# Kernel optimization log

Hardware: AMD Instinct MI355X
Metric: run time of the kernel (lower is better)

Reference implementation:

```python
import jax, jax.numpy as jnp
import numpy as np

B, T, C, H, N = 2, 1024, 2048, 32, 64
LAYER_ID, N_LAYERS = 12, 24
EPS = 1e-5 * 8 ** 2  # GroupNorm eps = 1e-5 * head_size_divisor**2


def setup_inputs() -> dict:
    key = jax.random.key(0)
    ks = jax.random.split(key, 16)
    nrm = lambda i, shape, s: jax.random.normal(ks[i], shape, jnp.float32) * s
    r01 = LAYER_ID / (N_LAYERS - 1)
    r1a0 = 1.0 - LAYER_ID / N_LAYERS
    ddd = (jnp.arange(C, dtype=jnp.float32) / C)[None, None, :]
    nn_ = jnp.arange(C, dtype=jnp.float32) / (C - 1)
    decay_speed = -7.0 + 5.0 * nn_ ** (0.85 + r01 ** 0.5)
    lin_s = 1.0 / float(np.sqrt(C))
    inp = dict(
        x=nrm(0, (B, T, C), 1.0),
        v_first=nrm(1, (B, T, C), 1.0),
        shift_state=jnp.zeros((B, C), jnp.float32),
        wkv_state=jnp.zeros((B, H, N, N), jnp.float32),
        x_r=1.0 - ddd ** (0.2 * r1a0),
        x_w=1.0 - ddd ** (0.9 * r1a0),
        x_k=1.0 - (ddd ** (0.9 * r1a0) + 0.4 * r01),
        x_v=1.0 - (ddd ** (0.4 * r1a0) + 0.6 * r01),
        x_a=1.0 - ddd ** (0.9 * r1a0),
        x_g=1.0 - ddd ** (0.2 * r1a0),
        w0=decay_speed[None, None, :] + 0.5,
        w1=nrm(2, (C, 64), 0.05), w2=nrm(3, (64, C), 0.1),
        a0=jnp.zeros((1, 1, C), jnp.float32),
        a1=nrm(4, (C, 64), 0.05), a2=nrm(5, (64, C), 0.1),
        v0=jnp.ones((1, 1, C), jnp.float32),
        v1=nrm(6, (C, 32), 0.05), v2=nrm(7, (32, C), 0.1),
        g1=nrm(8, (C, 128), 0.05), g2=nrm(9, (128, C), 0.1),
        k_k=jnp.full((1, 1, C), 0.85, jnp.float32),
        k_a=jnp.ones((1, 1, C), jnp.float32),
        r_k=nrm(10, (H, N), 0.02),
        W_r=nrm(11, (C, C), lin_s), W_k=nrm(12, (C, C), lin_s),
        W_v=nrm(13, (C, C), lin_s), W_o=nrm(14, (C, C), lin_s),
        ln_w=jnp.ones((C,), jnp.float32), ln_b=jnp.zeros((C,), jnp.float32),
    )
    return inp


def _forward(x, v_first, shift_state, wkv_state, x_r, x_w, x_k, x_v, x_a, x_g,
             w0, w1, w2, a0, a1, a2, v0, v1, v2, g1, g2, k_k, k_a, r_k,
             W_r, W_k, W_v, W_o, ln_w, ln_b):
    # token shift
    xx = jnp.concatenate([shift_state[:, None, :], x[:, :-1]], axis=1) - x
    xr, xw, xk, xv, xa, xg = (x + xx * m for m in (x_r, x_w, x_k, x_v, x_a, x_g))
    r = xr @ W_r
    k = xk @ W_k
    v = xv @ W_v
    # log-decay (strictly negative)
    w_log = -jax.nn.softplus(-(w0 + jnp.tanh(xw @ w1) @ w2)) - 0.5
    # residual value mixing towards layer-0 v (layer_id > 0 branch)
    v = v + (v_first - v) * jax.nn.sigmoid(v0 + xv @ v1 @ v2)
    a = jax.nn.sigmoid(a0 + xa @ a1 @ a2)
    g = jax.nn.sigmoid(xg @ g1) @ g2
    # per-head L2-normalized removal key
    kk = (k * k_k).reshape(B, T, H, N)
    kk = kk / jnp.maximum(jnp.linalg.norm(kk, axis=-1, keepdims=True), 1e-12)
    k2 = k * (1.0 + (a - 1.0) * k_a)
    # time-major [T,B,H,N] for the scan
    tm = lambda t: t.reshape(B, T, H, N).transpose(1, 0, 2, 3)
    rs, ks_, vs = tm(r), tm(k2), tm(v)
    ws = jnp.exp(tm(w_log))               # per-channel decay in (0,1)
    a_in = -kk.transpose(1, 0, 2, 3)      # removal direction
    b_in = (kk * a.reshape(B, T, H, N)).transpose(1, 0, 2, 3)
    def step(S, t):  # S: [B,H,Nv,Nk]
        r_, k_, v_, w_, a_, b_ = t
        sa = jnp.einsum('bhvk,bhk->bhv', S, a_)
        S = S * w_[:, :, None, :] \
            + jnp.einsum('bhv,bhk->bhvk', sa, b_) \
            + jnp.einsum('bhv,bhk->bhvk', v_, k_)
        return S, jnp.einsum('bhvk,bhk->bhv', S, r_)
    S_final, o = jax.lax.scan(step, wkv_state, (rs, ks_, vs, ws, a_in, b_in))
    o = o.transpose(1, 0, 2, 3)           # [B,T,H,N]
    # GroupNorm with H groups over C channels (per-head normalization)
    mu = o.mean(-1, keepdims=True)
    var = ((o - mu) ** 2).mean(-1, keepdims=True)
    on = ((o - mu) / jnp.sqrt(var + EPS)).reshape(B, T, C) * ln_w + ln_b
    # rkv bonus term
    rr, kr, vr = r.reshape(B, T, H, N), k2.reshape(B, T, H, N), v.reshape(B, T, H, N)
    bonus = ((rr * kr * r_k).sum(-1, keepdims=True) * vr).reshape(B, T, C)
    out = ((on + bonus) * g) @ W_o
    return out


def reference(x, v_first, shift_state, wkv_state, x_r, x_w, x_k, x_v, x_a, x_g,
              w0, w1, w2, a0, a1, a2, v0, v1, v2, g1, g2, k_k, k_a, r_k,
              W_r, W_k, W_v, W_o, ln_w, ln_b):
    return _forward(x, v_first, shift_state, wkv_state, x_r, x_w, x_k, x_v, x_a, x_g,
                    w0, w1, w2, a0, a1, a2, v0, v1, v2, g1, g2, k_k, k_a, r_k,
                    W_r, W_k, W_v, W_o, ln_w, ln_b)
```

## Files before the change

kernel.cpp:

```cpp
#include <hip/hip_runtime.h>
#include <cstdint>
#include <cstddef>


#define DI __device__ __forceinline__
static constexpr int T_ = 1024, C_ = 2048, H_ = 32;

typedef __attribute__((ext_vector_type(8))) __bf16 bf16x8;
typedef __attribute__((ext_vector_type(4))) float f32x4;
typedef __attribute__((ext_vector_type(8))) unsigned short us8v;
typedef __attribute__((ext_vector_type(4))) unsigned short us4v;
typedef __attribute__((ext_vector_type(2))) unsigned short us2v;

DI float sig_(float z) { return 1.0f / (1.0f + expf(-z)); }

DI unsigned short f2bf(float f) {
  union { float f; uint32_t u; } v; v.f = f;
  uint32_t u = v.u;
  return (unsigned short)((u + 0x7FFFu + ((u >> 16) & 1u)) >> 16);
}
DI float bf2f(unsigned short h) {
  union { uint32_t u; float f; } v; v.u = ((uint32_t)h) << 16;
  return v.f;
}

DI float dpp_xor1_add(float x) {
  int r = __builtin_amdgcn_update_dpp(0, __float_as_int(x), 0xB1, 0xF, 0xF, true);
  return x + __int_as_float(r);
}
DI float dpp_xor2_add(float x) {
  int r = __builtin_amdgcn_update_dpp(0, __float_as_int(x), 0x4E, 0xF, 0xF, true);
  return x + __int_as_float(r);
}
DI float dpp_hm_add(float x) {
  int r = __builtin_amdgcn_update_dpp(0, __float_as_int(x), 0x141, 0xF, 0xF, true);
  return x + __int_as_float(r);
}
DI float dpp_mir_add(float x) {
  int r = __builtin_amdgcn_update_dpp(0, __float_as_int(x), 0x140, 0xF, 0xF, true);
  return x + __int_as_float(r);
}

DI void gload16(const float* g, float* l) {
  __builtin_amdgcn_global_load_lds(
      (const __attribute__((address_space(1))) uint32_t*)g,
      (__attribute__((address_space(3))) uint32_t*)l, 16, 0, 0);
}
DI void gload16u(const unsigned short* g, unsigned short* l) {
  __builtin_amdgcn_global_load_lds(
      (const __attribute__((address_space(1))) uint32_t*)g,
      (__attribute__((address_space(3))) uint32_t*)l, 16, 0, 0);
}
DI void gload4(const float* g, float* l) {
  __builtin_amdgcn_global_load_lds(
      (const __attribute__((address_space(1))) uint32_t*)g,
      (__attribute__((address_space(3))) uint32_t*)l, 4, 0, 0);
}

struct Job {
  const float* A; const float* W; float* C; const float* bias;
  const float* mixv; const float* x; const float* shift;
  int N, K, ntn, aact, epi, tile_end;
};
struct Jobs { Job j[7]; };

__global__ __launch_bounds__(256) void gemm_oracle(Jobs P) {
  __shared__ float As[64][33];
  __shared__ float Ws[32][65];
  int bx = blockIdx.x, ji = 0;
  while (bx >= P.j[ji].tile_end) ++ji;
  Job J = P.j[ji];
  int tix = bx - (ji ? P.j[ji - 1].tile_end : 0);
  int mt = tix / J.ntn, nt = tix % J.ntn;
  int m0 = mt * 64, n0 = nt * 64;
  int tid = threadIdx.x, tx = tid & 15, ty = tid >> 4;
  float acc[4][4] = {};
  for (int k0 = 0; k0 < J.K; k0 += 32) {
    #pragma unroll
    for (int p = 0; p < 8; ++p) {
      int idx = p * 256 + tid;
      int r = idx >> 5, kc = idx & 31;
      int m = m0 + r, k = k0 + kc;
      float a;
      if (J.mixv) {
        float xv = J.x[(size_t)m * C_ + k];
        int t = m & (T_ - 1);
        float xp = (t == 0) ? J.shift[(size_t)(m >> 10) * C_ + k]
                            : J.x[(size_t)(m - 1) * C_ + k];
        a = xv + (xp - xv) * J.mixv[k];
      } else {
        a = J.A[(size_t)m * J.K + k];
        if (J.aact == 1) a = tanhf(a);
        else if (J.aact == 2) a = sig_(a);
      }
      As[r][kc] = a;
    }
    #pragma unroll
    for (int p = 0; p < 8; ++p) {
      int idx = p * 256 + tid;
      int kr = idx >> 6, nc = idx & 63;
      int n = n0 + nc;
      Ws[kr][nc] = (n < J.N) ? J.W[(size_t)(k0 + kr) * J.N + n] : 0.0f;
    }
    __syncthreads();
    #pragma unroll 4
    for (int kc = 0; kc < 32; ++kc) {
      float av[4], bv[4];
      #pragma unroll
      for (int i = 0; i < 4; ++i) av[i] = As[ty * 4 + i][kc];
      #pragma unroll
      for (int jn = 0; jn < 4; ++jn) bv[jn] = Ws[kc][tx * 4 + jn];
      #pragma unroll
      for (int i = 0; i < 4; ++i)
        #pragma unroll
        for (int jn = 0; jn < 4; ++jn) acc[i][jn] += av[i] * bv[jn];
    }
    __syncthreads();
  }
  #pragma unroll
  for (int i = 0; i < 4; ++i) {
    int rw = m0 + ty * 4 + i;
    #pragma unroll
    for (int jn = 0; jn < 4; ++jn) {
      int col = n0 + tx * 4 + jn;
      if (col < J.N) {
        float v = acc[i][jn];
        if (J.epi == 1) v = sig_(J.bias[col] + v);
        else if (J.epi == 2) v = 0.60653065971263342f * sig_(J.bias[col] + v);
        if (J.epi == 3) ((unsigned short*)J.C)[(size_t)rw * J.N + col] = f2bf(v);
        else            J.C[(size_t)rw * J.N + col] = v;
      }
    }
  }
}

struct TJob { const float* src; unsigned short* dh; unsigned short* dl; int N, ntn, tile_end; };
struct TJobs { TJob j[8]; };

__global__ __launch_bounds__(256) void wtrans(TJobs P) {
  __shared__ float t[64][65];
  int bx = blockIdx.x, ji = 0;
  while (bx >= P.j[ji].tile_end) ++ji;
  TJob J = P.j[ji];
  int tix = bx - (ji ? P.j[ji - 1].tile_end : 0);
  int kt = tix / J.ntn, nt = tix % J.ntn;
  int k0 = kt * 64, n0 = nt * 64;
  int tid = threadIdx.x;
  #pragma unroll
  for (int p = 0; p < 16; ++p) {
    int flat = p * 256 + tid;
    int r = flat >> 6, c = flat & 63;
    int n = n0 + c;
    t[r][c] = (n < J.N) ? J.src[(size_t)(k0 + r) * J.N + n] : 0.0f;
  }
  __syncthreads();
  #pragma unroll
  for (int p = 0; p < 8; ++p) {
    int flat = p * 256 + tid;
    int rr = flat >> 5, cc = (flat & 31) * 2;
    if (n0 + rr < J.N) {
      float w0v = t[cc][rr], w1v = t[cc + 1][rr];
      unsigned short h0 = f2bf(w0v), h1 = f2bf(w1v);
      us2v oh, ol;
      oh.x = h0; oh.y = h1;
      ol.x = f2bf(w0v - bf2f(h0));
      ol.y = f2bf(w1v - bf2f(h1));
      size_t off = (size_t)(n0 + rr) * 2048 + k0 + cc;
      *(us2v*)(J.dh + off) = oh;
      *(us2v*)(J.dl + off) = ol;
    }
  }
}

struct GJob {
  const float* A; const unsigned short* Wh; const unsigned short* Wl; float* C;
  const float* mixv; const float* shift;
  int N, K, ntn, kbeg, kend, atomicC, tile_end;
};
struct GJobs { GJob j[8]; };

__global__ __launch_bounds__(256, 2) void gemm_w256(GJobs P) {
  __shared__ unsigned short Ash[128][40];
  __shared__ unsigned short Asl[128][40];
  __shared__ unsigned short Bsh[256][32];
  __shared__ unsigned short Bsl[256][32];
  int bx = blockIdx.x, ji = 0;
  while (bx >= P.j[ji].tile_end) ++ji;
  GJob J = P.j[ji];
  int tix = bx - (ji ? P.j[ji - 1].tile_end : 0);
  int mt = tix / J.ntn, nt = tix % J.ntn;
  int m0 = mt * 128, n0 = nt * 256;
  int tid = threadIdx.x;
  int lane = tid & 63, wid = tid >> 6;
  int wr = wid >> 1, wc = wid & 1;
  int l15 = lane & 15, lg = lane >> 4;
  f32x4 acc[4][8] = {};

  int sr = tid >> 3, skq = tid & 7;
  float ax[4][4], aq[4][4], amv[4];

  auto loadA = [&](int k0) {
    int kk = k0 + skq * 4;
    if (J.mixv) *(float4*)amv = *(const float4*)(J.mixv + kk);
    #pragma unroll
    for (int p = 0; p < 4; ++p) {
      int m = m0 + p * 32 + sr;
      const float* xp0 = J.A + (size_t)m * J.K + kk;
      *(float4*)ax[p] = *(const float4*)xp0;
      if (J.mixv) {
        const float* pp = ((m & (T_ - 1)) == 0)
            ? (J.shift + (size_t)(m >> 10) * C_ + kk)
            : (xp0 - C_);
        *(float4*)aq[p] = *(const float4*)pp;
      }
    }
  };
  auto writeA = [&]() {
    #pragma unroll
    for (int p = 0; p < 4; ++p) {
      us4v oh, ol;
      #pragma unroll
      for (int q = 0; q < 4; ++q) {
        float va = J.mixv ? (ax[p][q] + (aq[p][q] - ax[p][q]) * amv[q]) : ax[p][q];
        unsigned short hq = f2bf(va);
        oh[q] = hq;
        ol[q] = f2bf(va - bf2f(hq));
      }
      int r = p * 32 + sr;
      *(us4v*)&Ash[r][skq * 4] = oh;
      *(us4v*)&Asl[r][skq * 4] = ol;
    }
  };
  auto stageB = [&](int k0) {
    #pragma unroll
    for (int j = 0; j < 4; ++j) {
      int r0 = wid * 64 + j * 16;
      int rdst = r0 + (lane >> 2);
      int nrow = n0 + rdst;
      if (nrow >= J.N) nrow = J.N - 1;
      int ssrc = (lane & 3) ^ ((rdst >> 1) & 3);
      size_t gofs = (size_t)nrow * J.K + k0 + ssrc * 8;
      gload16u(J.Wh + gofs, &Bsh[r0][0]);
      gload16u(J.Wl + gofs, &Bsl[r0][0]);
    }
  };

  loadA(J.kbeg);
  stageB(J.kbeg);
  writeA();
  asm volatile("s_waitcnt vmcnt(0)" ::: "memory");
  __syncthreads();

  for (int k0 = J.kbeg; k0 < J.kend; k0 += 32) {
    bool more = (k0 + 32 < J.kend);
    if (more) loadA(k0 + 32);
    bf16x8 afh[4], afl[4];
    #pragma unroll
    for (int i = 0; i < 4; ++i) {
      int rr = wr * 64 + i * 16 + l15;
      afh[i] = __builtin_bit_cast(bf16x8, *(const us8v*)&Ash[rr][lg * 8]);
      afl[i] = __builtin_bit_cast(bf16x8, *(const us8v*)&Asl[rr][lg * 8]);
    }
    #pragma unroll
    for (int jn = 0; jn < 8; ++jn) {
      int rb = wc * 128 + jn * 16 + l15;
      int sl = (lg ^ ((rb >> 1) & 3)) * 8;
      bf16x8 bh = __builtin_bit_cast(bf16x8, *(const us8v*)&Bsh[rb][sl]);
      bf16x8 bl = __builtin_bit_cast(bf16x8, *(const us8v*)&Bsl[rb][sl]);
      #pragma unroll
      for (int i = 0; i < 4; ++i) {
        acc[i][jn] = __builtin_amdgcn_mfma_f32_16x16x32_bf16(afh[i], bh, acc[i][jn], 0, 0, 0);
        acc[i][jn] = __builtin_amdgcn_mfma_f32_16x16x32_bf16(afl[i], bh, acc[i][jn], 0, 0, 0);
        acc[i][jn] = __builtin_amdgcn_mfma_f32_16x16x32_bf16(afh[i], bl, acc[i][jn], 0, 0, 0);
      }
    }
    __syncthreads();
    if (more) { stageB(k0 + 32); writeA(); }
    asm volatile("s_waitcnt vmcnt(0)" ::: "memory");
    __syncthreads();
  }

  int orow0 = m0 + wr * 64 + 4 * lg;
  int ocol0 = n0 + wc * 128 + l15;
  #pragma unroll
  for (int i = 0; i < 4; ++i) {
    #pragma unroll
    for (int jn = 0; jn < 8; ++jn) {
      int col = ocol0 + jn * 16;
      if (col < J.N) {
        #pragma unroll
        for (int rr = 0; rr < 4; ++rr) {
          size_t idx = (size_t)(orow0 + i * 16 + rr) * J.N + col;
          float v = acc[i][jn][rr];
          if (J.atomicC) atomicAdd(&J.C[idx], v);
          else           J.C[idx] = v;
        }
      }
    }
  }
}

__global__ __launch_bounds__(256) void prescan(
    float* __restrict__ kio, float* __restrict__ vio,
    float* __restrict__ amat_ain, float* __restrict__ vmix_bin,
    const float* __restrict__ vfirst,
    const float* __restrict__ k_k, const float* __restrict__ k_a) {
  int gh = blockIdx.x * 4 + (threadIdx.x >> 6);
  int lane = threadIdx.x & 63;
  int h = gh & (H_ - 1);
  size_t base = (size_t)gh * 64 + lane;
  int cc = h * 64 + lane;
  float kv = kio[base];
  float kkv = kv * k_k[cc];
  float ss = kkv * kkv;
  ss += __shfl_xor(ss, 1);  ss += __shfl_xor(ss, 2);  ss += __shfl_xor(ss, 4);
  ss += __shfl_xor(ss, 8);  ss += __shfl_xor(ss, 16); ss += __shfl_xor(ss, 32);
  float nrm = fmaxf(sqrtf(ss), 1e-12f);
  float kkn = kkv / nrm;
  float av = amat_ain[base];
  float vmv = vmix_bin[base];
  float vv = vio[base];
  kio[base] = kv * (1.0f + (av - 1.0f) * k_a[cc]);
  vio[base] = vv + (vfirst[base] - vv) * vmv;
  amat_ain[base] = -kkn;
  vmix_bin[base] = kkn * av;
}

static constexpr int CH = 8;
static constexpr int SEG = 512, WU = 96;

#define LOADSTEP(BUF, S_, Aa, Ww, Kk, Bb, Rr, Vt)                  \
  {                                                                \
    *(float4*)&Aa[0] = *(const float4*)&lds[BUF][3][S_][kb];       \
    *(float4*)&Ww[0] = *(const float4*)&lds[BUF][2][S_][kb];       \
    *(float4*)&Kk[0] = *(const float4*)&lds[BUF][1][S_][kb];       \
    *(float4*)&Bb[0] = *(const float4*)&lds[BUF][4][S_][kb];       \
    *(float4*)&Rr[0] = *(const float4*)&lds[BUF][0][S_][kb];       \
    Vt = vtl[BUF][S_][vr];                                         \
  }

#define COMPSTEP(Aa, Ww, Kk, Bb, Rr, Vt, TIDX)                              \
  {                                                                         \
    float p0 = S[0] * Aa[0], p1 = S[1] * Aa[1];                             \
    p0 = fmaf(S[2], Aa[2], p0);                                             \
    p1 = fmaf(S[3], Aa[3], p1);                                             \
    float sa = p0 + p1;                                                     \
    sa = dpp_xor1_add(sa);                                                  \
    sa = dpp_xor2_add(sa);                                                  \
    sa = dpp_hm_add(sa);                                                    \
    sa = dpp_mir_add(sa);                                                   \
    S[0] = fmaf(S[0], Ww[0], fmaf(Vt, Kk[0], sa * Bb[0]));                  \
    S[1] = fmaf(S[1], Ww[1], fmaf(Vt, Kk[1], sa * Bb[1]));                  \
    S[2] = fmaf(S[2], Ww[2], fmaf(Vt, Kk[2], sa * Bb[2]));                  \
    S[3] = fmaf(S[3], Ww[3], fmaf(Vt, Kk[3], sa * Bb[3]));                  \
    float y0 = S[0] * Rr[0], y1 = S[1] * Rr[1];                             \
    y0 = fmaf(S[2], Rr[2], y0);                                             \
    y1 = fmaf(S[3], Rr[3], y1);                                             \
    float y = y0 + y1;                                                      \
    y = dpp_xor1_add(y);                                                    \
    y = dpp_xor2_add(y);                                                    \
    y = dpp_hm_add(y);                                                      \
    y = dpp_mir_add(y);                                                     \
    if (kq == 0 && (TIDX) >= outfrom)                                       \
      obf[bh + (size_t)(TIDX)*2048 + v0 + vr] = f2bf(y);                    \
  }

__global__ __launch_bounds__(128) void wkv_scan_v8(
    const float* __restrict__ r, const float* __restrict__ k2,
    const float* __restrict__ w, const float* __restrict__ ain,
    const float* __restrict__ bin, const float* __restrict__ vp,
    const float* __restrict__ sInit, unsigned short* __restrict__ obf) {
  __shared__ float lds[2][5][CH][64];
  __shared__ float vtl[2][CH][8];
  int D = blockIdx.x;
  int chain = (D & 7) + 8 * (D >> 7);
  int inner = (D >> 3) & 15;
  int seg = inner >> 3, vpair = inner & 7;
  int b = chain >> 5, h = chain & 31;
  int v0 = vpair * 8;
  int tid = threadIdx.x;
  int wid = tid >> 6, lane = tid & 63;
  int vl = lane >> 4, kq = lane & 15;
  int kb = kq * 4;
  int vr = wid * 4 + vl;
  size_t bh = (size_t)(b * T_) * 2048 + (size_t)h * 64;

  float S[4];
  if (seg == 0) {
    const float* sp = sInit + (((size_t)chain * 64 + v0 + vr) * 64) + kb;
    float4 s0 = *(const float4*)sp;
    S[0] = s0.x; S[1] = s0.y; S[2] = s0.z; S[3] = s0.w;
  } else {
    S[0] = S[1] = S[2] = S[3] = 0.0f;
  }

  const float* arr[5] = {r, k2, w, ain, bin};

  auto stage = [&](int buf, int t0) {
    for (int d = wid; d < 10; d += 2) {
      int a = d >> 1, hf = d & 1;
      size_t gofs = bh + (size_t)(t0 + hf * 4 + (lane >> 4)) * 2048 + (lane & 15) * 4;
      gload16(arr[a] + gofs, &lds[buf][a][hf * 4][0]);
    }
    if (wid == 0) {
      size_t gofs = bh + (size_t)(t0 + (lane >> 3)) * 2048 + v0 + (lane & 7);
      gload4(vp + gofs, &vtl[buf][0][0]);
    }
  };

  int tstart = seg ? (SEG - WU) : 0;
  int nch = (seg ? (SEG + WU) : SEG) / CH;
  int outfrom = seg * SEG;

  stage(0, tstart);
  asm volatile("s_waitcnt vmcnt(0)" ::: "memory");
  __syncthreads();

  float A0[4], W0[4], K0[4], B0[4], R0[4], vt0;
  float A1[4], W1[4], K1[4], B1[4], R1[4], vt1;

  for (int c = 0; c < nch; ++c) {
    int cur = c & 1;
    int t0 = tstart + c * CH;
    if (c + 1 < nch) stage(cur ^ 1, t0 + CH);
    LOADSTEP(cur, 0, A0, W0, K0, B0, R0, vt0);
    #pragma unroll 2
    for (int s = 0; s < CH; s += 2) {
      LOADSTEP(cur, s + 1, A1, W1, K1, B1, R1, vt1);
      COMPSTEP(A0, W0, K0, B0, R0, vt0, t0 + s);
      if (s + 2 < CH) LOADSTEP(cur, s + 2, A0, W0, K0, B0, R0, vt0);
      COMPSTEP(A1, W1, K1, B1, R1, vt1, t0 + s + 1);
    }
    asm volatile("s_waitcnt vmcnt(0)" ::: "memory");
    __syncthreads();
  }
}

__global__ __launch_bounds__(256) void post(
    const unsigned short* __restrict__ obf, const float* __restrict__ r,
    const float* __restrict__ k2, const float* __restrict__ vp,
    const unsigned short* __restrict__ gbf, const float* __restrict__ r_k,
    const float* __restrict__ lnw, const float* __restrict__ lnb,
    float* __restrict__ afin) {
  int gh = blockIdx.x * 4 + (threadIdx.x >> 6);
  int lane = threadIdx.x & 63;
  int h = gh & 31;
  size_t base = (size_t)gh * 64 + lane;
  int cc = h * 64 + lane;
  float ov = bf2f(obf[base]);
  float pr = r[base] * k2[base] * r_k[cc];
  float so = ov, so2 = ov * ov, sd = pr;
  #pragma unroll
  for (int d = 1; d <= 32; d <<= 1) {
    so  += __shfl_xor(so, d);
    so2 += __shfl_xor(so2, d);
    sd  += __shfl_xor(sd, d);
  }
  float mu = so * (1.0f / 64.0f);
  float var = so2 * (1.0f / 64.0f) - mu * mu;
  float on = (ov - mu) * rsqrtf(var + 6.4e-4f) * lnw[cc] + lnb[cc];
  float val = (on + sd * vp[base]) * bf2f(gbf[base]);
  afin[base] = val;
}

static constexpr size_t KB = 1024;
static constexpr size_t O_R    = 0;
static constexpr size_t O_K    = 16384;
static constexpr size_t O_V    = 32768;
static constexpr size_t O_WDEC = 49152;
static constexpr size_t O_AMAT = 65536;
static constexpr size_t O_VMIX = 81920;
static constexpr size_t O_AIN  = O_AMAT;
static constexpr size_t O_BIN  = O_VMIX;
static constexpr size_t O_AFIN = O_VMIX;
static constexpr size_t O_WRT_H = 49152, O_WRT_L = 57344;
static constexpr size_t O_WKT_H = 65536, O_WKT_L = 73728;
static constexpr size_t O_WVT_H = 81920, O_WVT_L = 90112;
static constexpr size_t O_W1T_H = 98304, O_W1T_L = 98560;
static constexpr size_t O_A1T_H = 98816, O_A1T_L = 99072;
static constexpr size_t O_V1T_H = 99328, O_V1T_L = 99456;
static constexpr size_t O_G1T_H = 99584, O_G1T_L = 100096;
static constexpr size_t O_WOT_H = 0, O_WOT_L = 8192;

extern "C" void kernel_launch(void* const* d_in, const int* in_sizes, int n_in,
                              void* d_out, int out_size, void* d_ws, size_t ws_size,
                              hipStream_t stream) {
  const float* x      = (const float*)d_in[0];
  const float* vfirst = (const float*)d_in[1];
  const float* shift  = (const float*)d_in[2];
  const float* wkv0   = (const float*)d_in[3];
  const float* x_r = (const float*)d_in[4];
  const float* x_w = (const float*)d_in[5];
  const float* x_k = (const float*)d_in[6];
  const float* x_v = (const float*)d_in[7];
  const float* x_a = (const float*)d_in[8];
  const float* x_g = (const float*)d_in[9];
  const float* w0 = (const float*)d_in[10];
  const float* w1 = (const float*)d_in[11];
  const float* w2 = (const float*)d_in[12];
  const float* a0 = (const float*)d_in[13];
  const float* a1 = (const float*)d_in[14];
  const float* a2 = (const float*)d_in[15];
  const float* v0 = (const float*)d_in[16];
  const float* v1 = (const float*)d_in[17];
  const float* v2 = (const float*)d_in[18];
  const float* g1 = (const float*)d_in[19];
  const float* g2 = (const float*)d_in[20];
  const float* k_k = (const float*)d_in[21];
  const float* k_a = (const float*)d_in[22];
  const float* r_k = (const float*)d_in[23];
  const float* W_r = (const float*)d_in[24];
  const float* W_k = (const float*)d_in[25];
  const float* W_v = (const float*)d_in[26];
  const float* W_o = (const float*)d_in[27];
  const float* ln_w = (const float*)d_in[28];
  const float* ln_b = (const float*)d_in[29];

  char* ws = (char*)d_ws;
  auto F = [&](size_t kb) { return (float*)(ws + kb * KB); };
  auto U = [&](size_t kb) { return (unsigned short*)(ws + kb * KB); };
  float* outp = (float*)d_out;
  unsigned short* gbf = (unsigned short*)d_out;
  unsigned short* obf = (unsigned short*)((char*)d_out + 8192 * KB);
  float* HW2 = (float*)((char*)d_out + 8192 * KB);
  float* HA2 = (float*)((char*)d_out + 8704 * KB);
  float* HV2 = (float*)((char*)d_out + 9216 * KB);
  float* HG2 = (float*)((char*)d_out + 9472 * KB);

  {
    TJobs TG{};
    int cum = 0, i = 0;
    auto addT = [&](const float* src, size_t hkb, size_t lkb, int N) {
      int ntn = (N + 63) / 64;
      cum += 32 * ntn;
      TG.j[i++] = TJob{src, U(hkb), U(lkb), N, ntn, cum};
    };
    addT(W_r, O_WRT_H, O_WRT_L, 2048);
    addT(W_k, O_WKT_H, O_WKT_L, 2048);
    addT(W_v, O_WVT_H, O_WVT_L, 2048);
    addT(w1, O_W1T_H, O_W1T_L, 64);
    addT(a1, O_A1T_H, O_A1T_L, 64);
    addT(v1, O_V1T_H, O_V1T_L, 32);
    addT(g1, O_G1T_H, O_G1T_L, 128);
    wtrans<<<dim3(cum), dim3(256), 0, stream>>>(TG);
  }

  {
    GJobs G{};
    int cum = 0, i = 0;
    auto add = [&](size_t hkb, size_t lkb, float* Cp, const float* mixv, int N) {
      int ntn = (N + 255) / 256;
      cum += 16 * ntn;
      G.j[i++] = GJob{x, U(hkb), U(lkb), Cp, mixv, shift, N, 2048, ntn, 0, 2048, 0, cum};
    };
    add(O_WRT_H, O_WRT_L, F(O_R), x_r, 2048);
    add(O_WKT_H, O_WKT_L, F(O_K), x_k, 2048);
    add(O_WVT_H, O_WVT_L, F(O_V), x_v, 2048);
    add(O_W1T_H, O_W1T_L, HW2, x_w, 64);
    add(O_A1T_H, O_A1T_L, HA2, x_a, 64);
    add(O_V1T_H, O_V1T_L, HV2, x_v, 32);
    add(O_G1T_H, O_G1T_L, HG2, x_g, 128);
    gemm_w256<<<dim3(cum), dim3(256), 0, stream>>>(G);
  }

  {
    Jobs G{};
    int cum = 0, i = 0;
    auto add = [&](const float* A, const float* W, float* C, const float* bias,
                   int K, int aact, int epi) {
      cum += 32 * 32;
      G.j[i++] = Job{A, W, C, bias, nullptr, nullptr, nullptr, 2048, K, 32, aact, epi, cum};
    };
    add(HW2, w2, F(O_WDEC), w0, 64, 1, 2);
    add(HA2, a2, F(O_AMAT), a0, 64, 0, 1);
    add(HV2, v2, F(O_VMIX), v0, 32, 0, 1);
    add(HG2, g2, (float*)gbf, nullptr, 128, 2, 3);
    gemm_oracle<<<dim3(cum), dim3(256), 0, stream>>>(G);
  }

  prescan<<<dim3(16384), dim3(256), 0, stream>>>(F(O_K), F(O_V), F(O_AMAT), F(O_VMIX),
                                                 vfirst, k_k, k_a);

  wkv_scan_v8<<<dim3(1024), dim3(128), 0, stream>>>(F(O_R), F(O_K), F(O_WDEC), F(O_AIN),
                                                    F(O_BIN), F(O_V), wkv0, obf);

  post<<<dim3(16384), dim3(256), 0, stream>>>(obf, F(O_R), F(O_K), F(O_V),
                                              gbf, r_k, ln_w, ln_b, F(O_AFIN));

  hipMemsetAsync(d_out, 0, (size_t)16384 * KB, stream);

  {
    TJobs TO{};
    TO.j[0] = TJob{W_o, U(O_WOT_H), U(O_WOT_L), 2048, 32, 1024};
    wtrans<<<dim3(1024), dim3(256), 0, stream>>>(TO);
  }

  {
    GJobs G{};
    G.j[0] = GJob{F(O_AFIN), U(O_WOT_H), U(O_WOT_L), outp, nullptr, nullptr,
                  2048, 2048, 8, 0, 1024, 1, 128};
    G.j[1] = GJob{F(O_AFIN), U(O_WOT_H), U(O_WOT_L), outp, nullptr, nullptr,
                  2048, 2048, 8, 1024, 2048, 1, 256};
    gemm_w256<<<dim3(256), dim3(256), 0, stream>>>(G);
  }

  (void)in_sizes; (void)n_in; (void)out_size; (void)ws_size;
}
```

Before: 823.3 us.

## Route LoRA up-projections through split-bf16 MFMA GEMM with fused activations

Removes the scalar fp32 gemm_oracle kernel and runs the four small-K up-projections (w2, a2, v2, g2) on the split-bf16 MFMA gemm_w256 kernel. Their weights are now pre-transposed into hi/lo bf16 pairs by the shared wtrans launch, which gains a K bound. The tanh/sigmoid input activation and the bias-sigmoid/bf16 epilogues move into gemm_w256. The A-tile staging is reorganised to 8-wide vector stores into an XOR-swizzled, unpadded LDS layout, meant to avoid bank conflicts. The cost is more transpose work and scratch space borrowed in the output buffer, and every GEMM now carries extra per-element branches in staging and epilogue.

```diff
diff --git a/kernel.cpp b/kernel.cpp
--- a/kernel.cpp
+++ b/kernel.cpp
@@ -57,90 +57,14 @@
       (__attribute__((address_space(3))) uint32_t*)l, 4, 0, 0);
 }
 
-struct Job {
-  const float* A; const float* W; float* C; const float* bias;
-  const float* mixv; const float* x; const float* shift;
-  int N, K, ntn, aact, epi, tile_end;
-};
-struct Jobs { Job j[7]; };
-
-__global__ __launch_bounds__(256) void gemm_oracle(Jobs P) {
-  __shared__ float As[64][33];
-  __shared__ float Ws[32][65];
-  int bx = blockIdx.x, ji = 0;
-  while (bx >= P.j[ji].tile_end) ++ji;
-  Job J = P.j[ji];
-  int tix = bx - (ji ? P.j[ji - 1].tile_end : 0);
-  int mt = tix / J.ntn, nt = tix % J.ntn;
-  int m0 = mt * 64, n0 = nt * 64;
-  int tid = threadIdx.x, tx = tid & 15, ty = tid >> 4;
-  float acc[4][4] = {};
-  for (int k0 = 0; k0 < J.K; k0 += 32) {
-    #pragma unroll
-    for (int p = 0; p < 8; ++p) {
-      int idx = p * 256 + tid;
-      int r = idx >> 5, kc = idx & 31;
-      int m = m0 + r, k = k0 + kc;
-      float a;
-      if (J.mixv) {
-        float xv = J.x[(size_t)m * C_ + k];
-        int t = m & (T_ - 1);
-        float xp = (t == 0) ? J.shift[(size_t)(m >> 10) * C_ + k]
-                            : J.x[(size_t)(m - 1) * C_ + k];
-        a = xv + (xp - xv) * J.mixv[k];
-      } else {
-        a = J.A[(size_t)m * J.K + k];
-        if (J.aact == 1) a = tanhf(a);
-        else if (J.aact == 2) a = sig_(a);
-      }
-      As[r][kc] = a;
-    }
-    #pragma unroll
-    for (int p = 0; p < 8; ++p) {
-      int idx = p * 256 + tid;
-      int kr = idx >> 6, nc = idx & 63;
-      int n = n0 + nc;
-      Ws[kr][nc] = (n < J.N) ? J.W[(size_t)(k0 + kr) * J.N + n] : 0.0f;
-    }
-    __syncthreads();
-    #pragma unroll 4
-    for (int kc = 0; kc < 32; ++kc) {
-      float av[4], bv[4];
-      #pragma unroll
-      for (int i = 0; i < 4; ++i) av[i] = As[ty * 4 + i][kc];
-      #pragma unroll
-      for (int jn = 0; jn < 4; ++jn) bv[jn] = Ws[kc][tx * 4 + jn];
-      #pragma unroll
-      for (int i = 0; i < 4; ++i)
-        #pragma unroll
-        for (int jn = 0; jn < 4; ++jn) acc[i][jn] += av[i] * bv[jn];
-    }
-    __syncthreads();
-  }
-  #pragma unroll
-  for (int i = 0; i < 4; ++i) {
-    int rw = m0 + ty * 4 + i;
-    #pragma unroll
-    for (int jn = 0; jn < 4; ++jn) {
-      int col = n0 + tx * 4 + jn;
-      if (col < J.N) {
-        float v = acc[i][jn];
-        if (J.epi == 1) v = sig_(J.bias[col] + v);
-        else if (J.epi == 2) v = 0.60653065971263342f * sig_(J.bias[col] + v);
-        if (J.epi == 3) ((unsigned short*)J.C)[(size_t)rw * J.N + col] = f2bf(v);
-        else            J.C[(size_t)rw * J.N + col] = v;
-      }
-    }
-  }
-}
-
-struct TJob { const float* src; unsigned short* dh; unsigned short* dl; int N, ntn, tile_end; };
-struct TJobs { TJob j[8]; };
+struct TJob { const float* src; unsigned short* dh; unsigned short* dl;
+              int N, K, ntn, tile_end; };
+struct TJobs { TJob j[12]; };
 
 __global__ __launch_bounds__(256) void wtrans(TJobs P) {
   __shared__ float t[64][65];
   int bx = blockIdx.x, ji = 0;
-  while (bx >= P.j[ji].tile_end) ++ji;
+  while (ji < 11 && bx >= P.j[ji].tile_end) ++ji;
   TJob J = P.j[ji];
   int tix = bx - (ji ? P.j[ji - 1].tile_end : 0);
   int kt = tix / J.ntn, nt = tix % J.ntn;
@@ -151,21 +75,21 @@
     int flat = p * 256 + tid;
     int r = flat >> 6, c = flat & 63;
     int n = n0 + c;
-    t[r][c] = (n < J.N) ? J.src[(size_t)(k0 + r) * J.N + n] : 0.0f;
+    t[r][c] = (n < J.N && k0 + r < J.K) ? J.src[(size_t)(k0 + r) * J.N + n] : 0.0f;
   }
   __syncthreads();
   #pragma unroll
   for (int p = 0; p < 8; ++p) {
     int flat = p * 256 + tid;
     int rr = flat >> 5, cc = (flat & 31) * 2;
-    if (n0 + rr < J.N) {
+    if (n0 + rr < J.N && k0 + cc < J.K) {
       float w0v = t[cc][rr], w1v = t[cc + 1][rr];
       unsigned short h0 = f2bf(w0v), h1 = f2bf(w1v);
       us2v oh, ol;
       oh.x = h0; oh.y = h1;
       ol.x = f2bf(w0v - bf2f(h0));
       ol.y = f2bf(w1v - bf2f(h1));
-      size_t off = (size_t)(n0 + rr) * 2048 + k0 + cc;
+      size_t off = (size_t)(n0 + rr) * J.K + k0 + cc;
       *(us2v*)(J.dh + off) = oh;
       *(us2v*)(J.dl + off) = ol;
     }
@@ -174,18 +98,18 @@
 
 struct GJob {
   const float* A; const unsigned short* Wh; const unsigned short* Wl; float* C;
-  const float* mixv; const float* shift;
-  int N, K, ntn, kbeg, kend, atomicC, tile_end;
+  const float* mixv; const float* shift; const float* bias;
+  int N, K, ntn, kbeg, kend, atomicC, aact, epi, tile_end;
 };
 struct GJobs { GJob j[8]; };
 
 __global__ __launch_bounds__(256, 2) void gemm_w256(GJobs P) {
-  __shared__ unsigned short Ash[128][40];
-  __shared__ unsigned short Asl[128][40];
+  __shared__ unsigned short Ash[128][32];
+  __shared__ unsigned short Asl[128][32];
   __shared__ unsigned short Bsh[256][32];
   __shared__ unsigned short Bsl[256][32];
   int bx = blockIdx.x, ji = 0;
-  while (bx >= P.j[ji].tile_end) ++ji;
+  while (ji < 7 && bx >= P.j[ji].tile_end) ++ji;
   GJob J = P.j[ji];
   int tix = bx - (ji ? P.j[ji - 1].tile_end : 0);
   int mt = tix / J.ntn, nt = tix % J.ntn;
@@ -196,39 +120,48 @@
   int l15 = lane & 15, lg = lane >> 4;
   f32x4 acc[4][8] = {};
 
-  int sr = tid >> 3, skq = tid & 7;
-  float ax[4][4], aq[4][4], amv[4];
+  int sr4 = tid >> 2, sk8 = (tid & 3) * 8;
+  float ax[2][8], aq[2][8], amv[8];
 
   auto loadA = [&](int k0) {
-    int kk = k0 + skq * 4;
-    if (J.mixv) *(float4*)amv = *(const float4*)(J.mixv + kk);
+    int kk = k0 + sk8;
+    if (J.mixv) {
+      *(float4*)&amv[0] = *(const float4*)(J.mixv + kk);
+      *(float4*)&amv[4] = *(const float4*)(J.mixv + kk + 4);
+    }
     #pragma unroll
-    for (int p = 0; p < 4; ++p) {
-      int m = m0 + p * 32 + sr;
+    for (int p = 0; p < 2; ++p) {
+      int m = m0 + p * 64 + sr4;
       const float* xp0 = J.A + (size_t)m * J.K + kk;
-      *(float4*)ax[p] = *(const float4*)xp0;
+      *(float4*)&ax[p][0] = *(const float4*)xp0;
+      *(float4*)&ax[p][4] = *(const float4*)(xp0 + 4);
       if (J.mixv) {
         const float* pp = ((m & (T_ - 1)) == 0)
             ? (J.shift + (size_t)(m >> 10) * C_ + kk)
             : (xp0 - C_);
-        *(float4*)aq[p] = *(const float4*)pp;
+        *(float4*)&aq[p][0] = *(const float4*)pp;
+        *(float4*)&aq[p][4] = *(const float4*)(pp + 4);
       }
     }
   };
   auto writeA = [&]() {
     #pragma unroll
-    for (int p = 0; p < 4; ++p) {
-      us4v oh, ol;
+    for (int p = 0; p < 2; ++p) {
+      int r = p * 64 + sr4;
+      us8v oh, ol;
       #pragma unroll
-      for (int q = 0; q < 4; ++q) {
-        float va = J.mixv ? (ax[p][q] + (aq[p][q] - ax[p][q]) * amv[q]) : ax[p][q];
+      for (int q = 0; q < 8; ++q) {
+        float va = ax[p][q];
+        if (J.mixv) va = va + (aq[p][q] - va) * amv[q];
+        if (J.aact == 1) va = tanhf(va);
+        else if (J.aact == 2) va = sig_(va);
         unsigned short hq = f2bf(va);
         oh[q] = hq;
         ol[q] = f2bf(va - bf2f(hq));
       }
-      int r = p * 32 + sr;
-      *(us4v*)&Ash[r][skq * 4] = oh;
-      *(us4v*)&Asl[r][skq * 4] = ol;
+      int sp = ((tid & 3) ^ ((r >> 1) & 3)) * 8;
+      *(us8v*)&Ash[r][sp] = oh;
+      *(us8v*)&Asl[r][sp] = ol;
     }
   };
   auto stageB = [&](int k0) {
@@ -258,8 +191,9 @@
     #pragma unroll
     for (int i = 0; i < 4; ++i) {
       int rr = wr * 64 + i * 16 + l15;
-      afh[i] = __builtin_bit_cast(bf16x8, *(const us8v*)&Ash[rr][lg * 8]);
-      afl[i] = __builtin_bit_cast(bf16x8, *(const us8v*)&Asl[rr][lg * 8]);
+      int sa_ = (lg ^ ((rr >> 1) & 3)) * 8;
+      afh[i] = __builtin_bit_cast(bf16x8, *(const us8v*)&Ash[rr][sa_]);
+      afl[i] = __builtin_bit_cast(bf16x8, *(const us8v*)&Asl[rr][sa_]);
     }
     #pragma unroll
     for (int jn = 0; jn < 8; ++jn) {
@@ -292,8 +226,11 @@
         for (int rr = 0; rr < 4; ++rr) {
           size_t idx = (size_t)(orow0 + i * 16 + rr) * J.N + col;
           float v = acc[i][jn][rr];
-          if (J.atomicC) atomicAdd(&J.C[idx], v);
-          else           J.C[idx] = v;
+          if (J.epi == 1) v = sig_(J.bias[col] + v);
+          else if (J.epi == 2) v = 0.60653065971263342f * sig_(J.bias[col] + v);
+          if (J.atomicC)          atomicAdd(&J.C[idx], v);
+          else if (J.epi == 3)    ((unsigned short*)J.C)[idx] = f2bf(v);
+          else                    J.C[idx] = v;
         }
       }
     }
@@ -481,6 +418,10 @@
 static constexpr size_t O_V1T_H = 99328, O_V1T_L = 99456;
 static constexpr size_t O_G1T_H = 99584, O_G1T_L = 100096;
 static constexpr size_t O_WOT_H = 0, O_WOT_L = 8192;
+static constexpr size_t D_W2T_H = 10496, D_W2T_L = 10752;
+static constexpr size_t D_A2T_H = 11008, D_A2T_L = 11264;
+static constexpr size_t D_V2T_H = 11520, D_V2T_L = 11648;
+static constexpr size_t D_G2T_H = 11776, D_G2T_L = 12288;
 
 extern "C" void kernel_launch(void* const* d_in, const int* in_sizes, int n_in,
                               void* d_out, int out_size, void* d_ws, size_t ws_size,
@@ -519,6 +460,7 @@
   char* ws = (char*)d_ws;
   auto F = [&](size_t kb) { return (float*)(ws + kb * KB); };
   auto U = [&](size_t kb) { return (unsigned short*)(ws + kb * KB); };
+  auto D = [&](size_t kb) { return (unsigned short*)((char*)d_out + kb * KB); };
   float* outp = (float*)d_out;
   unsigned short* gbf = (unsigned short*)d_out;
   unsigned short* obf = (unsigned short*)((char*)d_out + 8192 * KB);
@@ -530,18 +472,23 @@
   {
     TJobs TG{};
     int cum = 0, i = 0;
-    auto addT = [&](const float* src, size_t hkb, size_t lkb, int N) {
+    auto addT = [&](const float* src, unsigned short* dh, unsigned short* dl,
+                    int N, int K) {
       int ntn = (N + 63) / 64;
-      cum += 32 * ntn;
-      TG.j[i++] = TJob{src, U(hkb), U(lkb), N, ntn, cum};
+      cum += ((K + 63) / 64) * ntn;
+      TG.j[i++] = TJob{src, dh, dl, N, K, ntn, cum};
     };
-    addT(W_r, O_WRT_H, O_WRT_L, 2048);
-    addT(W_k, O_WKT_H, O_WKT_L, 2048);
-    addT(W_v, O_WVT_H, O_WVT_L, 2048);
-    addT(w1, O_W1T_H, O_W1T_L, 64);
-    addT(a1, O_A1T_H, O_A1T_L, 64);
-    addT(v1, O_V1T_H, O_V1T_L, 32);
-    addT(g1, O_G1T_H, O_G1T_L, 128);
+    addT(W_r, U(O_WRT_H), U(O_WRT_L), 2048, 2048);
+    addT(W_k, U(O_WKT_H), U(O_WKT_L), 2048, 2048);
+    addT(W_v, U(O_WVT_H), U(O_WVT_L), 2048, 2048);
+    addT(w1, U(O_W1T_H), U(O_W1T_L), 64, 2048);
+    addT(a1, U(O_A1T_H), U(O_A1T_L), 64, 2048);
+    addT(v1, U(O_V1T_H), U(O_V1T_L), 32, 2048);
+    addT(g1, U(O_G1T_H), U(O_G1T_L), 128, 2048);
+    addT(w2, D(D_W2T_H), D(D_W2T_L), 2048, 64);
+    addT(a2, D(D_A2T_H), D(D_A2T_L), 2048, 64);
+    addT(v2, D(D_V2T_H), D(D_V2T_L), 2048, 32);
+    addT(g2, D(D_G2T_H), D(D_G2T_L), 2048, 128);
     wtrans<<<dim3(cum), dim3(256), 0, stream>>>(TG);
   }
 
@@ -551,7 +498,8 @@
     auto add = [&](size_t hkb, size_t lkb, float* Cp, const float* mixv, int N) {
       int ntn = (N + 255) / 256;
       cum += 16 * ntn;
-      G.j[i++] = GJob{x, U(hkb), U(lkb), Cp, mixv, shift, N, 2048, ntn, 0, 2048, 0, cum};
+      G.j[i++] = GJob{x, U(hkb), U(lkb), Cp, mixv, shift, nullptr,
+                      N, 2048, ntn, 0, 2048, 0, 0, 0, cum};
     };
     add(O_WRT_H, O_WRT_L, F(O_R), x_r, 2048);
     add(O_WKT_H, O_WKT_L, F(O_K), x_k, 2048);
@@ -564,18 +512,19 @@
   }
 
   {
-    Jobs G{};
+    GJobs G{};
     int cum = 0, i = 0;
-    auto add = [&](const float* A, const float* W, float* C, const float* bias,
-                   int K, int aact, int epi) {
-      cum += 32 * 32;
-      G.j[i++] = Job{A, W, C, bias, nullptr, nullptr, nullptr, 2048, K, 32, aact, epi, cum};
+    auto add = [&](const float* A, size_t whkb, size_t wlkb, float* Cp,
+                   const float* bias, int K, int aact, int epi) {
+      cum += 16 * 8;
+      G.j[i++] = GJob{A, D(whkb), D(wlkb), Cp, nullptr, nullptr, bias,
+                      2048, K, 8, 0, K, 0, aact, epi, cum};
     };
-    add(HW2, w2, F(O_WDEC), w0, 64, 1, 2);
-    add(HA2, a2, F(O_AMAT), a0, 64, 0, 1);
-    add(HV2, v2, F(O_VMIX), v0, 32, 0, 1);
-    add(HG2, g2, (float*)gbf, nullptr, 128, 2, 3);
-    gemm_oracle<<<dim3(cum), dim3(256), 0, stream>>>(G);
+    add(HW2, D_W2T_H, D_W2T_L, F(O_WDEC), w0, 64, 1, 2);
+    add(HA2, D_A2T_H, D_A2T_L, F(O_AMAT), a0, 64, 0, 1);
+    add(HV2, D_V2T_H, D_V2T_L, F(O_VMIX), v0, 32, 0, 1);
+    add(HG2, D_G2T_H, D_G2T_L, (float*)gbf, nullptr, 128, 2, 3);
+    gemm_w256<<<dim3(cum), dim3(256), 0, stream>>>(G);
   }
 
   prescan<<<dim3(16384), dim3(256), 0, stream>>>(F(O_K), F(O_V), F(O_AMAT), F(O_VMIX),
@@ -591,16 +540,16 @@
 
   {
     TJobs TO{};
-    TO.j[0] = TJob{W_o, U(O_WOT_H), U(O_WOT_L), 2048, 32, 1024};
+    TO.j[0] = TJob{W_o, U(O_WOT_H), U(O_WOT_L), 2048, 2048, 32, 1024};
     wtrans<<<dim3(1024), dim3(256), 0, stream>>>(TO);
   }
 
   {
     GJobs G{};
-    G.j[0] = GJob{F(O_AFIN), U(O_WOT_H), U(O_WOT_L), outp, nullptr, nullptr,
-                  2048, 2048, 8, 0, 1024, 1, 128};
-    G.j[1] = GJob{F(O_AFIN), U(O_WOT_H), U(O_WOT_L), outp, nullptr, nullptr,
-                  2048, 2048, 8, 1024, 2048, 1, 256};
+    G.j[0] = GJob{F(O_AFIN), U(O_WOT_H), U(O_WOT_L), outp, nullptr, nullptr, nullptr,
+                  2048, 2048, 8, 0, 1024, 1, 0, 0, 128};
+    G.j[1] = GJob{F(O_AFIN), U(O_WOT_H), U(O_WOT_L), outp, nullptr, nullptr, nullptr,
+                  2048, 2048, 8, 1024, 2048, 1, 0, 0, 256};
     gemm_w256<<<dim3(256), dim3(256), 0, stream>>>(G);
   }
 
```

New measurement: 827.9 us. No clear change (+0.6%).
